# Performance work log

Hardware: AMD Instinct MI355X
Metric: run time of the kernel (lower is better)

## Reference

```python
import jax, jax.numpy as jnp
import numpy as np
import math

IN_FEATURES = 4096
OUT_FEATURES = 4096
P = max(IN_FEATURES, OUT_FEATURES)   # total_permutations
D = min(IN_FEATURES, OUT_FEATURES)   # diag_length
SPARSITY = 0.1
K = math.ceil(int((1.0 - SPARSITY) * IN_FEATURES * OUT_FEATURES) / D)  # 3687
ALPHA_LR = 0.01
NUM_ITER = 50


def sparse_soft_topk_mask_dykstra(alpha, k, l, num_iter):
    """Dykstra projection of alpha/l onto {0<=m<=1, sum(m)=k} (soft top-k mask)."""
    s = alpha / l
    n = s.shape[0]
    p0 = jnp.zeros_like(s)
    q0 = jnp.zeros_like(s)

    def body(carry, _):
        x, p, q = carry
        # project x+p onto hyperplane sum = k
        t = x + p
        y = t + (k - jnp.sum(t)) / n
        p = t - y
        # project y+q onto box [0, 1]
        u = y + q
        x_new = jnp.clip(u, 0.0, 1.0)
        q = u - x_new
        return (x_new, p, q), None

    (x, _, _), _ = jax.lax.scan(body, (s, p0, q0), None, length=num_iter)
    return x  # last projection is onto the box -> exact zeros / ones


def compute_weight(V, alpha):
    a = sparse_soft_topk_mask_dykstra(alpha, K, ALPHA_LR, NUM_ITER)  # (P,)
    vals = a[:, None] * V                                             # (P, D)
    i = jnp.arange(P)[:, None]
    j = jnp.arange(D)[None, :]
    if OUT_FEATURES >= IN_FEATURES:
        # pseudo-diagonal i: rows shifted by i, column j scaled by V[i, j]
        rows = (i + j) % OUT_FEATURES
        cols = jnp.broadcast_to(j, (P, D))
    else:
        # row r scaled by V[i, r], columns shifted by i
        rows = jnp.broadcast_to(j, (P, D))
        cols = (i + j) % IN_FEATURES
    W = jnp.zeros((OUT_FEATURES, IN_FEATURES), V.dtype)
    W = W.at[rows.reshape(-1), cols.reshape(-1)].add(vals.reshape(-1))
    return W


def setup_inputs() -> dict:
    key = jax.random.key(0)
    k1, k2 = jax.random.split(key)
    # kaiming_uniform_(a=sqrt(5)) over fan_in = D -> bound = sqrt(1/D)
    bound = 1.0 / np.sqrt(D)
    V = jax.random.uniform(k1, (P, D), jnp.float32, -bound, bound)
    alpha = jnp.ones((P,), jnp.float32) / IN_FEATURES
    x = jax.random.normal(k2, (512, IN_FEATURES), jnp.float32)
    return {"x": x, "V": V, "alpha": alpha}


def reference(x, V, alpha):
    W = compute_weight(V, alpha)  # (out, in)
    return x @ W.T                # F.linear(x, W)
```

## Files before the change

kernel.cpp:

```cpp
#include <hip/hip_runtime.h>
#include <hip/hip_bf16.h>
#include <stdint.h>

#define PDIM 4096
#define KSEL 3687.0f
#define NITER 50

typedef unsigned short ushort_t;
typedef __attribute__((ext_vector_type(8))) __bf16 bf16x8;
typedef __attribute__((ext_vector_type(4))) float f32x4;

typedef __attribute__((address_space(3))) void lds_void;
typedef __attribute__((address_space(1))) const void glob_void;

__device__ __forceinline__ ushort_t f32_to_bf16_rne(float f) {
  union { float f; uint32_t u; } v; v.f = f;
  uint32_t r = 0x7FFFu + ((v.u >> 16) & 1u);
  return (ushort_t)((v.u + r) >> 16);
}

__device__ __forceinline__ float bf16_to_f32(ushort_t h) {
  union { uint32_t u; float f; } v; v.u = ((uint32_t)h) << 16;
  return v.f;
}

__device__ __forceinline__ void async_cp16(const void* g, void* l) {
  __builtin_amdgcn_global_load_lds((glob_void*)g, (lds_void*)l, 16, 0, 0);
}

__device__ __forceinline__ void raw_barrier() {
  __builtin_amdgcn_sched_barrier(0);
  asm volatile("" ::: "memory");
  __builtin_amdgcn_s_barrier();
  asm volatile("" ::: "memory");
  __builtin_amdgcn_sched_barrier(0);
}

__device__ __forceinline__ float wave_sum_dpp(float x) {
  float s = x;
  int t;
  t = __builtin_amdgcn_update_dpp(0, __float_as_int(s), 0x111, 0xF, 0xF, true);
  s += __int_as_float(t);
  t = __builtin_amdgcn_update_dpp(0, __float_as_int(s), 0x112, 0xF, 0xF, true);
  s += __int_as_float(t);
  t = __builtin_amdgcn_update_dpp(0, __float_as_int(s), 0x114, 0xF, 0xF, true);
  s += __int_as_float(t);
  t = __builtin_amdgcn_update_dpp(0, __float_as_int(s), 0x118, 0xF, 0xF, true);
  s += __int_as_float(t);
  t = __builtin_amdgcn_update_dpp(0, __float_as_int(s), 0x142, 0xA, 0xF, true);
  s += __int_as_float(t);
  t = __builtin_amdgcn_update_dpp(0, __float_as_int(s), 0x143, 0xC, 0xF, true);
  s += __int_as_float(t);
  return s;
}

__global__ __launch_bounds__(256) void prep_kernel(
    const float* __restrict__ alpha, float* __restrict__ a_out,
    const float* __restrict__ x, ushort_t* __restrict__ Xb, int n4,
    const float* __restrict__ V) {
  if (blockIdx.x >= 1 && blockIdx.x <= 2048) {
    const float4* V4 = (const float4*)V;
    const int base = (blockIdx.x - 1) * 2048 + (int)threadIdx.x;
#pragma unroll
    for (int i = 0; i < 8; ++i) {
      const float4 vv = V4[base + i * 256];
      asm volatile("" :: "v"(vv.x), "v"(vv.y), "v"(vv.z), "v"(vv.w));
    }
    return;
  }
  if (blockIdx.x != 0) {
    const int i = (blockIdx.x - 2049) * 256 + threadIdx.x;
    if (i < n4) {
      const float4 v = ((const float4*)x)[i];
      ushort4 o;
      o.x = f32_to_bf16_rne(v.x);
      o.y = f32_to_bf16_rne(v.y);
      o.z = f32_to_bf16_rne(v.z);
      o.w = f32_to_bf16_rne(v.w);
      ((ushort4*)Xb)[i] = o;
    }
    return;
  }
  __shared__ float red[8];
  const int tid = threadIdx.x;
  const int lane = tid & 63;
  const int wv = tid >> 6;
  float xx[16], q[16];
  float p = 0.0f;
#pragma unroll
  for (int i = 0; i < 16; ++i) {
    xx[i] = alpha[i * 256 + tid] * 100.0f;
    q[i] = 0.0f;
  }
  for (int it = 0; it < NITER; ++it) {
    float t[16];
    float loc = 0.0f;
#pragma unroll
    for (int i = 0; i < 16; ++i) { t[i] = xx[i] + p; loc += t[i]; }
    loc = wave_sum_dpp(loc);
    const int slot = (it & 1) * 4;
    if (lane == 63) red[slot + wv] = loc;
    __syncthreads();
    const float tot = red[slot] + red[slot + 1] + red[slot + 2] + red[slot + 3];
    const float corr = (KSEL - tot) * (1.0f / 4096.0f);
    p = -corr;
#pragma unroll
    for (int i = 0; i < 16; ++i) {
      const float y = t[i] + corr;
      const float u = y + q[i];
      const float xn = fminf(fmaxf(u, 0.0f), 1.0f);
      q[i] = u - xn;
      xx[i] = xn;
    }
  }
#pragma unroll
  for (int i = 0; i < 16; ++i) a_out[i * 256 + tid] = xx[i];
}

__global__ __launch_bounds__(256) void wmat_kernel(
    const float* __restrict__ V, const float* __restrict__ a,
    ushort_t* __restrict__ Wb) {
  __shared__ float vt[192][67];
  const int t = threadIdx.x;
  const int r0 = blockIdx.x * 128;
  const int c0 = blockIdx.y * 64;
  const int dbase = (r0 - c0 - 63 + 2 * PDIM) & (PDIM - 1);
  const int csub = (t & 15) * 4;
  const int rsub = t >> 4;
#pragma unroll
  for (int i = 0; i < 12; ++i) {
    const int ld = i * 16 + rsub;
    const int d = (dbase + ld) & (PDIM - 1);
    const float av = a[d];
    const float4 vv = *(const float4*)(V + (size_t)d * PDIM + c0 + csub);
    vt[ld][csub + 0] = av * vv.x;
    vt[ld][csub + 1] = av * vv.y;
    vt[ld][csub + 2] = av * vv.z;
    vt[ld][csub + 3] = av * vv.w;
  }
  __syncthreads();
#pragma unroll
  for (int k = 0; k < 4; ++k) {
    const int ry = (t >> 3) + k * 32;
    const int cb = (t & 7) * 8;
    ushort_t pk[8];
#pragma unroll
    for (int j = 0; j < 8; ++j) {
      const int c = cb + j;
      pk[j] = f32_to_bf16_rne(vt[ry - c + 63][c]);
    }
    *(uint4*)(Wb + (size_t)(r0 + ry) * PDIM + c0 + cb) = *(const uint4*)pk;
  }
}

__global__ __launch_bounds__(512, 2) void gemm_kernel(
    const ushort_t* __restrict__ Xb, const ushort_t* __restrict__ Wb,
    ushort_t* __restrict__ par) {
  constexpr int Kdim = 4096, KQ = 512, NIT = KQ / 64;
  __shared__ __align__(16) ushort_t As[2][256 * 64];
  __shared__ __align__(16) ushort_t Bs[2][256 * 64];
  const int tid = threadIdx.x;
  const int lane = tid & 63;
  const int w = tid >> 6;
  const int l15 = lane & 15;
  const int quad = lane >> 4;
  const int wr = w >> 2;
  const int wc = w & 3;
  const int bid = blockIdx.x;
  const int u = (bid & 7) * 32 + (bid >> 3);
  const int z = u & 7;
  const int tile = u >> 3;
  const int mblk = tile & 1;
  const int nblk = tile >> 1;
  const int m0 = mblk * 256;
  const int n0 = nblk * 256;
  const int kbase = z * KQ;
  const int crow8 = lane >> 3;
  const int slotj = lane & 7;

  f32x4 acc[8][4];
#pragma unroll
  for (int mt = 0; mt < 8; ++mt)
#pragma unroll
    for (int nt = 0; nt < 4; ++nt) acc[mt][nt] = (f32x4){0.f, 0.f, 0.f, 0.f};

  auto stage_half = [&](int buf, int it, int q) {
    const int k0 = kbase + it * 64;
    const int half = q & 1;
#pragma unroll
    for (int L = 0; L < 2; ++L) {
      const int chunk = half * 16 + L * 8 + w;
      const int row = chunk * 8 + crow8;
      const int j = slotj ^ (row & 7);
      if (q < 2)
        async_cp16(Xb + (size_t)(m0 + row) * Kdim + k0 + j * 8,
                   (char*)&As[buf][0] + (size_t)chunk * 1024);
      else
        async_cp16(Wb + (size_t)(n0 + row) * Kdim + k0 + j * 8,
                   (char*)&Bs[buf][0] + (size_t)chunk * 1024);
    }
  };

#pragma unroll
  for (int q = 0; q < 4; ++q) stage_half(0, 0, q);
  asm volatile("s_waitcnt vmcnt(0)" ::: "memory");
  raw_barrier();

  for (int t = 0; t < NIT; ++t) {
    const int cur = t & 1;
    const ushort_t* __restrict__ Ab = &As[cur][0];
    const ushort_t* __restrict__ Bb = &Bs[cur][0];
    bf16x8 bfr[4][2];
#pragma unroll
    for (int q = 0; q < 4; ++q) {
      if (t + 1 < NIT) stage_half(cur ^ 1, t + 1, q);
      if (q == 0) {
#pragma unroll
        for (int nt = 0; nt < 4; ++nt)
#pragma unroll
          for (int k2 = 0; k2 < 2; ++k2) {
            const int row = wc * 64 + nt * 16 + l15;
            const int cj = k2 * 4 + quad;
            bfr[nt][k2] =
                *(const bf16x8*)&Bb[(row * 8 + (cj ^ (row & 7))) * 8];
          }
      }
      bf16x8 afr[2][2];
#pragma unroll
      for (int mi = 0; mi < 2; ++mi)
#pragma unroll
        for (int k2 = 0; k2 < 2; ++k2) {
          const int row = wr * 128 + (q * 2 + mi) * 16 + l15;
          const int cj = k2 * 4 + quad;
          afr[mi][k2] = *(const bf16x8*)&Ab[(row * 8 + (cj ^ (row & 7))) * 8];
        }
      raw_barrier();
      asm volatile("s_waitcnt lgkmcnt(0)" ::: "memory");
      __builtin_amdgcn_sched_barrier(0);
      __builtin_amdgcn_s_setprio(1);
#pragma unroll
      for (int mi = 0; mi < 2; ++mi)
#pragma unroll
        for (int nt = 0; nt < 4; ++nt) {
          acc[q * 2 + mi][nt] = __builtin_amdgcn_mfma_f32_16x16x32_bf16(
              afr[mi][0], bfr[nt][0], acc[q * 2 + mi][nt], 0, 0, 0);
          acc[q * 2 + mi][nt] = __builtin_amdgcn_mfma_f32_16x16x32_bf16(
              afr[mi][1], bfr[nt][1], acc[q * 2 + mi][nt], 0, 0, 0);
        }
      __builtin_amdgcn_s_setprio(0);
      if (q == 3) asm volatile("s_waitcnt vmcnt(0)" ::: "memory");
      raw_barrier();
    }
  }
  ushort_t* pbase = par + ((size_t)z * 32 + tile) * 65536;
#pragma unroll
  for (int mt = 0; mt < 8; ++mt) {
#pragma unroll
    for (int nt = 0; nt < 4; ++nt) {
      const int slot = mt * 4 + nt;
      ushort4 o;
      o.x = f32_to_bf16_rne(acc[mt][nt][0]);
      o.y = f32_to_bf16_rne(acc[mt][nt][1]);
      o.z = f32_to_bf16_rne(acc[mt][nt][2]);
      o.w = f32_to_bf16_rne(acc[mt][nt][3]);
      *(ushort4*)(pbase + (size_t)(slot * 512 + tid) * 4) = o;
    }
  }
}

__global__ __launch_bounds__(512) void combine_kernel(
    const ushort_t* __restrict__ par, float* __restrict__ out) {
  const int tile = blockIdx.x >> 2;
  const int qh = blockIdx.x & 3;
  const int mblk = tile & 1;
  const int nblk = tile >> 1;
  const int m0 = mblk * 256;
  const int n0 = nblk * 256;
  const int tid = threadIdx.x;
  const int lane = tid & 63;
  const int w = tid >> 6;
  const int wr = w >> 2;
  const int wc = w & 3;
  const int l15 = lane & 15;
  const int quad = lane >> 4;
#pragma unroll
  for (int ss = 0; ss < 8; ++ss) {
    const int slot = qh * 8 + ss;
    float s0 = 0.f, s1 = 0.f, s2 = 0.f, s3 = 0.f;
#pragma unroll
    for (int z = 0; z < 8; ++z) {
      const ushort4 v = *(const ushort4*)(par +
          ((size_t)z * 32 + tile) * 65536 + (size_t)(slot * 512 + tid) * 4);
      s0 += bf16_to_f32(v.x);
      s1 += bf16_to_f32(v.y);
      s2 += bf16_to_f32(v.z);
      s3 += bf16_to_f32(v.w);
    }
    const int mt = slot >> 2;
    const int nt = slot & 3;
    const int mb = m0 + wr * 128 + mt * 16 + quad * 4;
    const int n = n0 + wc * 64 + nt * 16 + l15;
    out[(size_t)(mb + 0) * PDIM + n] = s0;
    out[(size_t)(mb + 1) * PDIM + n] = s1;
    out[(size_t)(mb + 2) * PDIM + n] = s2;
    out[(size_t)(mb + 3) * PDIM + n] = s3;
  }
}

extern "C" void kernel_launch(void* const* d_in, const int* in_sizes, int n_in,
                              void* d_out, int out_size, void* d_ws,
                              size_t ws_size, hipStream_t stream) {
  const float* x = (const float*)d_in[0];
  const float* V = (const float*)d_in[1];
  const float* alpha = (const float*)d_in[2];
  float* out = (float*)d_out;
  const int M = in_sizes[0] / PDIM;

  float* a_mask = (float*)d_ws;
  ushort_t* Xb = (ushort_t*)((char*)d_ws + 16 * 1024);
  ushort_t* Wb = Xb + (size_t)M * PDIM;
  ushort_t* par = Wb + (size_t)PDIM * PDIM;

  const int n4x = (M * PDIM) / 4;
  prep_kernel<<<1 + 2048 + (n4x + 255) / 256, 256, 0, stream>>>(
      alpha, a_mask, x, Xb, n4x, V);
  wmat_kernel<<<dim3(PDIM / 128, PDIM / 64), 256, 0, stream>>>(V, a_mask, Wb);
  gemm_kernel<<<256, 512, 0, stream>>>(Xb, Wb, par);
  combine_kernel<<<128, 512, 0, stream>>>(par, out);
}
```

Baseline: 155.8 us.

## Reorder GEMM K-loop into quadrant units with serpentine order and partial vmcnt waits

Reorganizes the main GEMM loop so each sub-step computes a 4x2 quadrant of the warp tile, loading A and B fragments per quadrant, and walks quadrants in serpentine order across iterations. Prefetch staging is split into four A/B units and issued in an order aligned with which LDS region becomes free. The full vmcnt(0) drain per iteration is replaced by partial vmcnt(4) waits, so global loads stay in flight longer. The cost is more LDS fragment reads per step and fragile wait-count bookkeeping that could race if the counts do not match the issued copies.

```diff
diff --git a/kernel.cpp b/kernel.cpp
--- a/kernel.cpp
+++ b/kernel.cpp
@@ -184,25 +184,38 @@
 #pragma unroll
     for (int nt = 0; nt < 4; ++nt) acc[mt][nt] = (f32x4){0.f, 0.f, 0.f, 0.f};
 
-  auto stage_half = [&](int buf, int it, int q) {
+  auto stageA = [&](int buf, int it, int h) {
     const int k0 = kbase + it * 64;
-    const int half = q & 1;
 #pragma unroll
     for (int L = 0; L < 2; ++L) {
-      const int chunk = half * 16 + L * 8 + w;
+      const int chunk = L * 16 + h * 8 + w;
       const int row = chunk * 8 + crow8;
       const int j = slotj ^ (row & 7);
-      if (q < 2)
-        async_cp16(Xb + (size_t)(m0 + row) * Kdim + k0 + j * 8,
-                   (char*)&As[buf][0] + (size_t)chunk * 1024);
-      else
-        async_cp16(Wb + (size_t)(n0 + row) * Kdim + k0 + j * 8,
-                   (char*)&Bs[buf][0] + (size_t)chunk * 1024);
+      async_cp16(Xb + (size_t)(m0 + row) * Kdim + k0 + j * 8,
+                 (char*)&As[buf][0] + (size_t)chunk * 1024);
     }
   };
-
-#pragma unroll
-  for (int q = 0; q < 4; ++q) stage_half(0, 0, q);
+  auto stageB = [&](int buf, int it, int h) {
+    const int k0 = kbase + it * 64;
+#pragma unroll
+    for (int L = 0; L < 2; ++L) {
+      const int idx = L * 8 + w;
+      const int chunk = (idx >> 2) * 8 + h * 4 + (idx & 3);
+      const int row = chunk * 8 + crow8;
+      const int j = slotj ^ (row & 7);
+      async_cp16(Wb + (size_t)(n0 + row) * Kdim + k0 + j * 8,
+                 (char*)&Bs[buf][0] + (size_t)chunk * 1024);
+    }
+  };
+  auto stage_unit = [&](int buf, int it, int u4) {
+    if (u4 < 2) stageA(buf, it, u4);
+    else stageB(buf, it, u4 - 2);
+  };
+
+  stage_unit(0, 0, 0);
+  stage_unit(0, 0, 2);
+  stage_unit(0, 0, 3);
+  stage_unit(0, 0, 1);
   asm volatile("s_waitcnt vmcnt(0)" ::: "memory");
   raw_barrier();
 
@@ -210,45 +223,58 @@
     const int cur = t & 1;
     const ushort_t* __restrict__ Ab = &As[cur][0];
     const ushort_t* __restrict__ Bb = &Bs[cur][0];
-    bf16x8 bfr[4][2];
 #pragma unroll
     for (int q = 0; q < 4; ++q) {
-      if (t + 1 < NIT) stage_half(cur ^ 1, t + 1, q);
-      if (q == 0) {
-#pragma unroll
-        for (int nt = 0; nt < 4; ++nt)
-#pragma unroll
-          for (int k2 = 0; k2 < 2; ++k2) {
-            const int row = wc * 64 + nt * 16 + l15;
-            const int cj = k2 * 4 + quad;
-            bfr[nt][k2] =
-                *(const bf16x8*)&Bb[(row * 8 + (cj ^ (row & 7))) * 8];
-          }
-      }
-      bf16x8 afr[2][2];
-#pragma unroll
-      for (int mi = 0; mi < 2; ++mi)
+      const int qq = (t & 1) ? (3 - q) : q;
+      const int mh = qq >> 1;
+      const int nh = qq & 1;
+      bf16x8 afr[4][2];
+      bf16x8 bfr[2][2];
+#pragma unroll
+      for (int mi = 0; mi < 4; ++mi)
 #pragma unroll
         for (int k2 = 0; k2 < 2; ++k2) {
-          const int row = wr * 128 + (q * 2 + mi) * 16 + l15;
+          const int row = wr * 128 + (mh * 4 + mi) * 16 + l15;
           const int cj = k2 * 4 + quad;
           afr[mi][k2] = *(const bf16x8*)&Ab[(row * 8 + (cj ^ (row & 7))) * 8];
         }
+#pragma unroll
+      for (int ni = 0; ni < 2; ++ni)
+#pragma unroll
+        for (int k2 = 0; k2 < 2; ++k2) {
+          const int row = wc * 64 + (nh * 2 + ni) * 16 + l15;
+          const int cj = k2 * 4 + quad;
+          bfr[ni][k2] = *(const bf16x8*)&Bb[(row * 8 + (cj ^ (row & 7))) * 8];
+        }
+      if (t + 1 < NIT) {
+        const int evst[4] = {1, 3, 2, 0};
+        const int odst[4] = {0, 2, 3, 1};
+        stage_unit(cur ^ 1, t + 1, (t & 1) ? odst[q] : evst[q]);
+      }
       raw_barrier();
+      if (t == NIT - 1) {
+        if (q == 0) asm volatile("s_waitcnt vmcnt(2)" ::: "memory");
+        else if (q == 1) asm volatile("s_waitcnt vmcnt(0)" ::: "memory");
+      } else {
+        asm volatile("s_waitcnt vmcnt(4)" ::: "memory");
+      }
       asm volatile("s_waitcnt lgkmcnt(0)" ::: "memory");
       __builtin_amdgcn_sched_barrier(0);
       __builtin_amdgcn_s_setprio(1);
 #pragma unroll
-      for (int mi = 0; mi < 2; ++mi)
-#pragma unroll
-        for (int nt = 0; nt < 4; ++nt) {
-          acc[q * 2 + mi][nt] = __builtin_amdgcn_mfma_f32_16x16x32_bf16(
-              afr[mi][0], bfr[nt][0], acc[q * 2 + mi][nt], 0, 0, 0);
-          acc[q * 2 + mi][nt] = __builtin_amdgcn_mfma_f32_16x16x32_bf16(
-              afr[mi][1], bfr[nt][1], acc[q * 2 + mi][nt], 0, 0, 0);
+      for (int mi = 0; mi < 4; ++mi)
+#pragma unroll
+        for (int ni = 0; ni < 2; ++ni) {
+          acc[mh * 4 + mi][nh * 2 + ni] =
+              __builtin_amdgcn_mfma_f32_16x16x32_bf16(
+                  afr[mi][0], bfr[ni][0], acc[mh * 4 + mi][nh * 2 + ni],
+                  0, 0, 0);
+          acc[mh * 4 + mi][nh * 2 + ni] =
+              __builtin_amdgcn_mfma_f32_16x16x32_bf16(
+                  afr[mi][1], bfr[ni][1], acc[mh * 4 + mi][nh * 2 + ni],
+                  0, 0, 0);
         }
       __builtin_amdgcn_s_setprio(0);
-      if (q == 3) asm volatile("s_waitcnt vmcnt(0)" ::: "memory");
       raw_barrier();
     }
   }
```

Measured after the change: 154.9 us. Within noise of the previous version (-0.6%).
